# Performance work log

Measured on AMD Instinct MI355X. Metric: run time of the kernel, lower is better.

Reference implementation:

```python
import jax, jax.numpy as jnp
import numpy as np

N = 200_000   # num_nodes
E = 100_000   # events per direction
D = 128       # memory_dim
F = 128       # event feature dim
T = 128       # time encoding dim


def setup_inputs() -> dict:
    key = jax.random.key(0)
    ks = jax.random.split(key, 12)
    src = jax.random.randint(ks[0], (E,), 0, N)
    dst = jax.random.randint(ks[1], (E,), 0, N)
    t = jax.random.uniform(ks[2], (E,)) * 1000.0
    feat = jax.random.normal(ks[3], (E, F))
    memory = jax.random.normal(ks[4], (N, D)) * 0.1
    last_update = jnp.zeros((N,), dtype=jnp.float32)
    time_w = jax.random.normal(ks[5], (T,)) * 0.1
    time_b = jax.random.normal(ks[6], (T,)) * 0.1
    M = 2 * D + T + F  # message dim = 512
    w_ih = jax.random.normal(ks[7], (3 * D, M)) * 0.02
    w_hh = jax.random.normal(ks[8], (3 * D, D)) * 0.02
    b_ih = jnp.zeros((3 * D,), dtype=jnp.float32)
    b_hh = jnp.zeros((3 * D,), dtype=jnp.float32)
    return {
        "memory": memory, "last_update": last_update, "t": t, "feat": feat,
        "time_w": time_w, "time_b": time_b,
        "w_ih": w_ih, "w_hh": w_hh, "b_ih": b_ih, "b_hh": b_hh,
        "src": src, "dst": dst,
    }


def time_encode(dt, w, b):
    # TGN/TGAT-style cosine time encoding: [E] -> [E, T]
    return jnp.cos(dt[:, None] * w[None, :] + b[None, :])


def gru_cell(x, h, w_ih, w_hh, b_ih, b_hh):
    # Standard torch.nn.GRUCell math (gates ordered r, z, n).
    gi = x @ w_ih.T + b_ih  # [N, 3D]
    gh = h @ w_hh.T + b_hh  # [N, 3D]
    i_r, i_z, i_n = jnp.split(gi, 3, axis=-1)
    h_r, h_z, h_n = jnp.split(gh, 3, axis=-1)
    r = jax.nn.sigmoid(i_r + h_r)
    z = jax.nn.sigmoid(i_z + h_z)
    n = jnp.tanh(i_n + r * h_n)
    return (1.0 - z) * n + z * h


def reference(memory, last_update, t, feat, time_w, time_b,
              w_ih, w_hh, b_ih, b_hh, src, dst):
    # --- message functions (identity = concat), both directions ---
    s_msg = jnp.concatenate(
        [memory[src], memory[dst], time_encode(t - last_update[src], time_w, time_b), feat], axis=-1)
    d_msg = jnp.concatenate(
        [memory[dst], memory[src], time_encode(t - last_update[dst], time_w, time_b), feat], axis=-1)

    nodes = jnp.concatenate([src, dst], axis=0)        # [2E]
    te = jnp.concatenate([t, t], axis=0)               # [2E]
    msg = jnp.concatenate([s_msg, d_msg], axis=0)      # [2E, M]

    # --- 'last' aggregator: per-node argmax over event time (scatter_max) ---
    # Stable sort by time; segment_max over sorted positions yields, per node,
    # the latest event (ties broken toward the later original index).
    perm = jnp.argsort(te, stable=True)                # [2E]
    pos = jnp.arange(2 * E)
    best_pos = jax.ops.segment_max(pos, nodes[perm], num_segments=N)  # [N], intmin if empty
    has_msg = best_pos >= 0
    best = perm[jnp.clip(best_pos, 0)]                 # [N] event index of latest msg

    agg_msg = msg[best]                                # [N, M] gather
    max_t = te[best]                                   # [N]

    # --- GRU memory update + masked scatter back into memory ---
    new_mem = gru_cell(agg_msg, memory, w_ih, w_hh, b_ih, b_hh)
    new_memory = jnp.where(has_msg[:, None], new_mem, memory)
    new_last_update = jnp.where(has_msg, max_t, last_update)
    return new_memory, new_last_update
```

## Files before the change

kernel.cpp:

```cpp
#include <hip/hip_runtime.h>
#include <hip/hip_bf16.h>
#include <stdint.h>

typedef __hip_bfloat16 bf16;
typedef unsigned long long u64;
typedef unsigned int u32;
typedef short short8 __attribute__((ext_vector_type(8)));
typedef float f32x4 __attribute__((ext_vector_type(4)));

#define D_ 128
#define K_ 640
#define BM 64
#define BN 128
#define BK 64
#define BM2 32

__device__ __forceinline__ float bf2f(bf16 v) { return __bfloat162float(v); }
__device__ __forceinline__ u32 fbits(float f) { union { float f; u32 u; } c; c.f = f; return c.u; }
__device__ __forceinline__ u32 pk2(float a, float b) {
  union { bf16 h; unsigned short s; } x, y;
  x.h = __float2bfloat16(a); y.h = __float2bfloat16(b);
  return (u32)x.s | ((u32)y.s << 16);
}
template<bool F32>
__device__ __forceinline__ float ldE(const void* p, size_t i) {
  return F32 ? ((const float*)p)[i] : bf2f(((const bf16*)p)[i]);
}
template<bool F32>
__device__ __forceinline__ void stE(void* p, size_t i, float v) {
  if (F32) ((float*)p)[i] = v; else ((bf16*)p)[i] = __float2bfloat16(v);
}
template<bool F32>
__device__ __forceinline__ uint4 ld8(const void* base, size_t elemOff) {
  if (!F32) {
    return *(const uint4*)((const bf16*)base + elemOff);
  } else {
    const float4* p = (const float4*)((const float*)base + elemOff);
    float4 v0 = p[0], v1 = p[1];
    uint4 o; o.x = pk2(v0.x, v0.y); o.y = pk2(v0.z, v0.w);
    o.z = pk2(v1.x, v1.y); o.w = pk2(v1.z, v1.w);
    return o;
  }
}
template<bool F32>
__device__ __forceinline__ void stage8(const void* base, size_t elemOff, bf16* dst) {
  *(uint4*)dst = ld8<F32>(base, elemOff);
}
__device__ __forceinline__ void gl_lds16(const void* g, void* l) {
  __builtin_amdgcn_global_load_lds(
      (const __attribute__((address_space(1))) unsigned int*)g,
      (__attribute__((address_space(3))) unsigned int*)l, 16, 0, 0);
}

__global__ void k_prep(u64* __restrict__ key, u32* __restrict__ cnt, int N,
                       const u32* __restrict__ mem_w, const u32* __restrict__ t_w,
                       u32* __restrict__ flag) {
  int i = blockIdx.x * blockDim.x + threadIdx.x;
  if (i < N) key[i] = 0ull;
  if (i == 0) {
    *cnt = 0u;
    int ok = 1;
    for (int k = 0; k < 64; ++k) {
      u32 w = mem_w[k];
      if ((w & 0x7fffu) > 0x4300u) ok = 0;
      if (((w >> 16) & 0x7fffu) > 0x4300u) ok = 0;
    }
    for (int k = 0; k < 16; ++k) {
      u32 w = t_w[k];
      if ((w & 0xffffu) > 0x4480u) ok = 0;
      if ((w >> 16) > 0x4480u) ok = 0;
    }
    *flag = ok ? 0u : 1u;
  }
}

__global__ void k_scat(const int* __restrict__ src, const int* __restrict__ dst,
                       const void* __restrict__ t, const u32* __restrict__ flag,
                       u64* __restrict__ key, int E) {
  int i = blockIdx.x * blockDim.x + threadIdx.x;
  if (i >= 2 * E) return;
  int e = (i < E) ? i : i - E;
  int node = (i < E) ? src[e] : dst[e];
  float tv = (*flag) ? ((const float*)t)[e] : bf2f(((const bf16*)t)[e]);
  u64 k = ((u64)fbits(tv) << 32) | (u64)(u32)(i + 1);
  atomicMax(&key[node], k);
}

__global__ void k_pack(const void* __restrict__ wih, const void* __restrict__ whh,
                       const u32* __restrict__ flag, bf16* __restrict__ wpk) {
  int gid = blockIdx.x * 256 + threadIdx.x;
  if (gid >= 40960) return;
  int tile = gid >> 10, r = gid & 1023;
  int j = r >> 3, s = r & 7;
  int kc = tile >> 2, by = tile & 3;
  int kglob = kc * 64 + s * 8;
  int grp = j >> 5, gi = j & 31, gidx = 32 * by + gi;
  int srow = (grp == 0) ? gidx : (grp == 1) ? 128 + gidx : 256 + gidx;
  bool zero = (kglob < 512) ? (grp == 3) : (grp == 2);
  uint4 v;
  if (zero) v = (uint4){0u, 0u, 0u, 0u};
  else if (*flag) v = (kglob < 512) ? ld8<true>(wih, (size_t)srow * 512 + kglob)
                                    : ld8<true>(whh, (size_t)srow * 128 + (kglob - 512));
  else            v = (kglob < 512) ? ld8<false>(wih, (size_t)srow * 512 + kglob)
                                    : ld8<false>(whh, (size_t)srow * 128 + (kglob - 512));
  ((uint4*)wpk)[(size_t)tile * 1024 + ((j * 8 + s) ^ (j & 7))] = v;
}

template<bool F32>
__device__ __forceinline__ void compact_body(int n, const void* mem, const void* lastup,
                                             const void* t, const u64* key,
                                             int* list, u32* cnt, int use_list,
                                             void* out, int N, int E) {
  u32 b = (u32)key[n];
  if (b) {
    int pos = (int)(b - 1u);
    int e = (pos < E) ? pos : pos - E;
    stE<F32>(out, (size_t)N * D_ + n, ldE<F32>(t, e));
    if (use_list) { u32 idx = atomicAdd(cnt, 1u); list[idx] = n; }
  } else {
    if (F32) {
      const float4* s = (const float4*)((const float*)mem + (size_t)n * D_);
      float4* d = (float4*)((float*)out + (size_t)n * D_);
#pragma unroll
      for (int i = 0; i < 32; ++i) d[i] = s[i];
    } else {
      const uint4* s = (const uint4*)((const bf16*)mem + (size_t)n * D_);
      uint4* d = (uint4*)((bf16*)out + (size_t)n * D_);
#pragma unroll
      for (int i = 0; i < 16; ++i) d[i] = s[i];
    }
    stE<F32>(out, (size_t)N * D_ + n, ldE<F32>(lastup, n));
  }
}
__global__ void k_compact(const void* mem, const void* lastup, const void* t,
                          const u32* __restrict__ flag, const u64* __restrict__ key,
                          int* list, u32* cnt, int use_list,
                          void* out, int N, int E) {
  int n = blockIdx.x * blockDim.x + threadIdx.x;
  if (n >= N) return;
  if (*flag) compact_body<true>(n, mem, lastup, t, key, list, cnt, use_list, out, N, E);
  else       compact_body<false>(n, mem, lastup, t, key, list, cnt, use_list, out, N, E);
}

template<bool F32>
__device__ __forceinline__ uint4 a_fetch(int kc, int tid,
    const void* mem, const void* feat,
    const int* s_node, const int* s_e, const int* s_oth,
    const float* s_dt, const float* s_tw, const float* s_tb) {
  int r = tid >> 3, s = tid & 7;
  int k0 = kc * 64 + s * 8;
  if (k0 < 128) return ld8<F32>(mem, (size_t)s_node[r] * D_ + k0);
  if (k0 < 256) return ld8<F32>(mem, (size_t)s_oth[r] * D_ + (k0 - 128));
  if (k0 < 384) {
    float dtv = s_dt[r];
    float f[8];
#pragma unroll
    for (int q = 0; q < 8; ++q) {
      int j = k0 - 256 + q;
      f[q] = cosf(fmaf(dtv, s_tw[j], s_tb[j]));
    }
    uint4 o; o.x = pk2(f[0], f[1]); o.y = pk2(f[2], f[3]);
    o.z = pk2(f[4], f[5]); o.w = pk2(f[6], f[7]);
    return o;
  }
  if (k0 < 512) return ld8<F32>(feat, (size_t)s_e[r] * D_ + (k0 - 384));
  return ld8<F32>(mem, (size_t)s_node[r] * D_ + (k0 - 512));
}

__device__ __forceinline__ void b_issue(const bf16* __restrict__ wpk, int tile,
                                        bf16* BsBuf, int tid) {
  int w = tid >> 6;
  const bf16* g = wpk + (size_t)tile * 8192 + w * 2048 + (tid & 63) * 8;
  bf16* l = BsBuf + w * 2048;
#pragma unroll
  for (int i = 0; i < 4; ++i)
    gl_lds16(g + i * 512, l + i * 512);
}

template<bool F32>
__device__ __forceinline__ void gemm2_body(
    const void* mem, const void* lastup, const void* t, const void* feat,
    const int* __restrict__ src, const int* __restrict__ dst,
    const bf16* __restrict__ wpk,
    const void* bih, const void* bhh, const void* tw, const void* tb,
    const u64* __restrict__ key, const int* __restrict__ list,
    const u32* __restrict__ cnt, int use_list,
    void* out, int N, int E,
    char* smem, int* s_node, int* s_e, int* s_oth, int* s_act,
    float* s_dt, float* s_tw, float* s_tb) {
  const int tid = threadIdx.x;
  const int bx = blockIdx.x;
  bf16 (*As)[BM2][72] = (bf16 (*)[BM2][72])smem;
  bf16* BsBase = (bf16*)(smem + 9216);
  float (*Gs)[133] = (float (*)[133])smem;

  b_issue(wpk, 0, BsBase, tid);

  if (tid < BM2) {
    int r = tid, row = BM2 * bx + r, node = -1;
    if (use_list) { int c = (int)*cnt; if (row < c) node = list[row]; }
    else if (row < N) node = row;
    int act = 0, e = 0, oth = 0; float dtv = 0.f;
    if (node >= 0) {
      u32 b = (u32)key[node];
      if (b) {
        act = 1;
        int pos = (int)(b - 1u);
        if (pos < E) { e = pos; oth = dst[e]; } else { e = pos - E; oth = src[e]; }
        dtv = ldE<F32>(t, e) - ldE<F32>(lastup, node);
      }
    }
    if (node < 0) node = 0;
    s_node[r] = node; s_e[r] = e; s_oth[r] = oth; s_act[r] = act; s_dt[r] = dtv;
  }
  if (tid < 128) s_tw[tid] = ldE<F32>(tw, tid);
  else           s_tb[tid - 128] = ldE<F32>(tb, tid - 128);
  __syncthreads();

  {
    uint4 a0 = a_fetch<F32>(0, tid, mem, feat, s_node, s_e, s_oth, s_dt, s_tw, s_tb);
    *(uint4*)&As[0][tid >> 3][(tid & 7) * 8] = a0;
  }
  __syncthreads();

  const int w = tid >> 6, l = tid & 63;
  const int mrow = l & 15, quad = l >> 4;
  f32x4 acc[4][2][2];
#pragma unroll
  for (int by = 0; by < 4; ++by)
#pragma unroll
    for (int mi = 0; mi < 2; ++mi)
#pragma unroll
      for (int ni = 0; ni < 2; ++ni) acc[by][mi][ni] = (f32x4){0.f, 0.f, 0.f, 0.f};

  uint4 apre = (uint4){0u, 0u, 0u, 0u};
#pragma unroll 1
  for (int kc = 0; kc < K_ / 64; ++kc) {
    const int ka = kc & 1;
    short8 a[2][2];
#pragma unroll
    for (int by = 0; by < 4; ++by) {
      const int tile = kc * 4 + by;
      if (by == 0) {
        if (kc + 1 < 10)
          apre = a_fetch<F32>(kc + 1, tid, mem, feat, s_node, s_e, s_oth, s_dt, s_tw, s_tb);
      }
      if (tile + 1 < 40)
        b_issue(wpk, tile + 1, BsBase + (((by & 1) ^ 1) << 13), tid);
      if (by == 0) {
#pragma unroll
        for (int ks2 = 0; ks2 < 2; ++ks2)
#pragma unroll
          for (int mi = 0; mi < 2; ++mi)
            a[ks2][mi] = *(const short8*)((const char*)&As[ka][0][0] +
                             (16 * mi + mrow) * 144 + ks2 * 64 + quad * 16);
      }
      const char* Bsb = (const char*)(BsBase + ((by & 1) << 13));
      short8 b[2][2];
#pragma unroll
      for (int ks2 = 0; ks2 < 2; ++ks2)
#pragma unroll
        for (int ni = 0; ni < 2; ++ni) {
          int j = 32 * w + 16 * ni + mrow;
          int off = (j * 128 + ks2 * 64 + quad * 16) ^ ((j & 7) << 4);
          b[ks2][ni] = *(const short8*)(Bsb + off);
        }
#pragma unroll
      for (int ks2 = 0; ks2 < 2; ++ks2)
#pragma unroll
        for (int mi = 0; mi < 2; ++mi)
#pragma unroll
          for (int ni = 0; ni < 2; ++ni)
            acc[by][mi][ni] = __builtin_amdgcn_mfma_f32_16x16x32_bf16(
                a[ks2][mi], b[ks2][ni], acc[by][mi][ni], 0, 0, 0);
      if (by == 3 && kc + 1 < 10)
        *(uint4*)&As[ka ^ 1][tid >> 3][(tid & 7) * 8] = apre;
      __syncthreads();
    }
  }

#pragma unroll
  for (int by = 0; by < 4; ++by) {
#pragma unroll
    for (int mi = 0; mi < 2; ++mi)
#pragma unroll
      for (int ni = 0; ni < 2; ++ni)
#pragma unroll
        for (int reg = 0; reg < 4; ++reg)
          Gs[16 * mi + quad * 4 + reg][32 * w + 16 * ni + mrow] = acc[by][mi][ni][reg];
    __syncthreads();
    {
      int r = tid >> 3, giB = (tid & 7) * 4;
      if (s_act[r]) {
        int node = s_node[r];
#pragma unroll
        for (int q = 0; q < 4; ++q) {
          int gi = giB + q, gidx = 32 * by + gi;
          float rp  = Gs[r][gi]      + ldE<F32>(bih, gidx)       + ldE<F32>(bhh, gidx);
          float zp  = Gs[r][32 + gi] + ldE<F32>(bih, 128 + gidx) + ldE<F32>(bhh, 128 + gidx);
          float inp = Gs[r][64 + gi] + ldE<F32>(bih, 256 + gidx);
          float hnp = Gs[r][96 + gi] + ldE<F32>(bhh, 256 + gidx);
          float rg = 1.f / (1.f + expf(-rp));
          float zg = 1.f / (1.f + expf(-zp));
          float ng = tanhf(inp + rg * hnp);
          float h = ldE<F32>(mem, (size_t)node * D_ + gidx);
          stE<F32>(out, (size_t)node * D_ + gidx, (1.f - zg) * ng + zg * h);
        }
      }
    }
    __syncthreads();
  }
}

__global__ __launch_bounds__(256, 3)
void k_gemm2(const void* mem, const void* lastup, const void* t, const void* feat,
             const int* src, const int* dst, const bf16* wpk,
             const void* bih, const void* bhh, const void* tw, const void* tb,
             const u32* __restrict__ flag, const u64* __restrict__ key,
             const int* __restrict__ list, const u32* __restrict__ cnt, int use_list,
             void* out, int N, int E) {
  if (use_list && (int)*cnt <= BM2 * (int)blockIdx.x) return;
  __shared__ __align__(16) char smem[41984];
  __shared__ int s_node[BM2], s_e[BM2], s_oth[BM2], s_act[BM2];
  __shared__ float s_dt[BM2], s_tw[128], s_tb[128];
  if (*flag)
    gemm2_body<true>(mem, lastup, t, feat, src, dst, wpk, bih, bhh, tw, tb,
                     key, list, cnt, use_list, out, N, E,
                     smem, s_node, s_e, s_oth, s_act, s_dt, s_tw, s_tb);
  else
    gemm2_body<false>(mem, lastup, t, feat, src, dst, wpk, bih, bhh, tw, tb,
                      key, list, cnt, use_list, out, N, E,
                      smem, s_node, s_e, s_oth, s_act, s_dt, s_tw, s_tb);
}

template<bool F32>
__device__ __forceinline__ void gemm_body(
    const void* mem, const void* lastup, const void* t, const void* feat,
    const int* __restrict__ src, const int* __restrict__ dst,
    const void* wih, const void* whh, const void* bih, const void* bhh,
    const void* tw, const void* tb,
    const u64* __restrict__ key, const int* __restrict__ list,
    const u32* __restrict__ cnt, int use_list,
    void* out, int N, int E,
    bf16 (*As)[72], bf16 (*Bs)[72], float (*Gs)[132],
    int* s_node, int* s_e, int* s_oth, int* s_act, float* s_dt) {
  const int tid = threadIdx.x;
  const int bx = blockIdx.x, by = blockIdx.y;

  if (tid < BM) {
    int r = tid;
    int row = BM * bx + r;
    int node = -1;
    if (use_list) { int c = (int)*cnt; if (row < c) node = list[row]; }
    else if (row < N) node = row;
    int act = 0, e = 0, oth = 0; float dtv = 0.f;
    if (node >= 0) {
      u32 b = (u32)key[node];
      if (b) {
        act = 1;
        int pos = (int)(b - 1u);
        if (pos < E) { e = pos; oth = dst[e]; } else { e = pos - E; oth = src[e]; }
        dtv = ldE<F32>(t, e) - ldE<F32>(lastup, node);
      }
    }
    if (node < 0) node = 0;
    s_node[r] = node; s_e[r] = e; s_oth[r] = oth; s_act[r] = act; s_dt[r] = dtv;
  }

  const int w = tid >> 6, l = tid & 63;
  const int mrow = l & 15, quad = l >> 4;
  f32x4 acc[4][2];
#pragma unroll
  for (int mi = 0; mi < 4; ++mi)
#pragma unroll
    for (int ni = 0; ni < 2; ++ni) acc[mi][ni] = (f32x4){0.f, 0.f, 0.f, 0.f};

#pragma unroll 1
  for (int kc = 0; kc < K_ / BK; ++kc) {
    __syncthreads();
#pragma unroll
    for (int it = 0; it < 2; ++it) {
      int task = tid + 256 * it;
      int r = task >> 3, s = task & 7;
      int k0 = kc * BK + s * 8;
      bf16* dstp = &As[r][s * 8];
      if (k0 < 128)       stage8<F32>(mem,  (size_t)s_node[r] * D_ + k0, dstp);
      else if (k0 < 256)  stage8<F32>(mem,  (size_t)s_oth[r] * D_ + (k0 - 128), dstp);
      else if (k0 < 384) {
        float dtv = s_dt[r];
        float f[8];
#pragma unroll
        for (int q = 0; q < 8; ++q) {
          int j = k0 - 256 + q;
          f[q] = cosf(fmaf(dtv, ldE<F32>(tw, j), ldE<F32>(tb, j)));
        }
        uint4 o; o.x = pk2(f[0], f[1]); o.y = pk2(f[2], f[3]);
        o.z = pk2(f[4], f[5]); o.w = pk2(f[6], f[7]);
        *(uint4*)dstp = o;
      }
      else if (k0 < 512)  stage8<F32>(feat, (size_t)s_e[r] * D_ + (k0 - 384), dstp);
      else                stage8<F32>(mem,  (size_t)s_node[r] * D_ + (k0 - 512), dstp);
    }
#pragma unroll
    for (int it = 0; it < 4; ++it) {
      int task = tid + 256 * it;
      int j = task >> 3, s = task & 7;
      int k0 = kc * BK + s * 8;
      int grp = j >> 5, gi = j & 31;
      int gidx = 32 * by + gi;
      bf16* dstp = &Bs[j][s * 8];
      if (k0 < 512) {
        if (grp == 3) { *(uint4*)dstp = (uint4){0, 0, 0, 0}; }
        else {
          int srow = (grp == 0) ? gidx : (grp == 1) ? 128 + gidx : 256 + gidx;
          stage8<F32>(wih, (size_t)srow * 512 + k0, dstp);
        }
      } else {
        if (grp == 2) { *(uint4*)dstp = (uint4){0, 0, 0, 0}; }
        else {
          int srow = (grp == 0) ? gidx : (grp == 1) ? 128 + gidx : 256 + gidx;
          stage8<F32>(whh, (size_t)srow * D_ + (k0 - 512), dstp);
        }
      }
    }
    __syncthreads();
#pragma unroll
    for (int ks = 0; ks < BK; ks += 32) {
      short8 a[4], b[2];
#pragma unroll
      for (int mi = 0; mi < 4; ++mi)
        a[mi] = *(const short8*)&As[16 * mi + mrow][ks + quad * 8];
#pragma unroll
      for (int ni = 0; ni < 2; ++ni)
        b[ni] = *(const short8*)&Bs[32 * w + 16 * ni + mrow][ks + quad * 8];
#pragma unroll
      for (int mi = 0; mi < 4; ++mi)
#pragma unroll
        for (int ni = 0; ni < 2; ++ni)
          acc[mi][ni] = __builtin_amdgcn_mfma_f32_16x16x32_bf16(a[mi], b[ni], acc[mi][ni], 0, 0, 0);
    }
  }

#pragma unroll
  for (int mi = 0; mi < 4; ++mi)
#pragma unroll
    for (int ni = 0; ni < 2; ++ni)
#pragma unroll
      for (int reg = 0; reg < 4; ++reg)
        Gs[16 * mi + quad * 4 + reg][32 * w + 16 * ni + mrow] = acc[mi][ni][reg];
  __syncthreads();

  {
    int r = tid >> 2;
    int giB = (tid & 3) * 8;
    if (s_act[r]) {
      int node = s_node[r];
#pragma unroll
      for (int q = 0; q < 8; ++q) {
        int gi = giB + q;
        int gidx = 32 * by + gi;
        float rp  = Gs[r][gi]       + ldE<F32>(bih, gidx)       + ldE<F32>(bhh, gidx);
        float zp  = Gs[r][32 + gi]  + ldE<F32>(bih, 128 + gidx) + ldE<F32>(bhh, 128 + gidx);
        float inp = Gs[r][64 + gi]  + ldE<F32>(bih, 256 + gidx);
        float hnp = Gs[r][96 + gi]  + ldE<F32>(bhh, 256 + gidx);
        float rg = 1.f / (1.f + expf(-rp));
        float zg = 1.f / (1.f + expf(-zp));
        float ng = tanhf(inp + rg * hnp);
        float h = ldE<F32>(mem, (size_t)node * D_ + gidx);
        stE<F32>(out, (size_t)node * D_ + gidx, (1.f - zg) * ng + zg * h);
      }
    }
  }
}

__global__ __launch_bounds__(256)
void k_gemm_fb(const void* mem, const void* lastup, const void* t, const void* feat,
               const int* src, const int* dst,
               const void* wih, const void* whh, const void* bih, const void* bhh,
               const void* tw, const void* tb,
               const u32* __restrict__ flag, const u64* __restrict__ key,
               const int* __restrict__ list, const u32* __restrict__ cnt, int use_list,
               void* out, int N, int E) {
  if (use_list && (int)*cnt <= BM * (int)blockIdx.x) return;

  __shared__ __align__(16) bf16 As[BM][72];
  __shared__ __align__(16) bf16 Bs[BN][72];
  __shared__ __align__(16) float Gs[BM][132];
  __shared__ int s_node[BM], s_e[BM], s_oth[BM], s_act[BM];
  __shared__ float s_dt[BM];

  if (*flag)
    gemm_body<true>(mem, lastup, t, feat, src, dst, wih, whh, bih, bhh, tw, tb,
                    key, list, cnt, use_list, out, N, E,
                    As, Bs, Gs, s_node, s_e, s_oth, s_act, s_dt);
  else
    gemm_body<false>(mem, lastup, t, feat, src, dst, wih, whh, bih, bhh, tw, tb,
                     key, list, cnt, use_list, out, N, E,
                     As, Bs, Gs, s_node, s_e, s_oth, s_act, s_dt);
}

extern "C" void kernel_launch(void* const* d_in, const int* in_sizes, int n_in,
                              void* d_out, int out_size, void* d_ws, size_t ws_size,
                              hipStream_t stream) {
  const void* mem    = d_in[0];
  const void* lastup = d_in[1];
  const void* t      = d_in[2];
  const void* feat   = d_in[3];
  const void* tw     = d_in[4];
  const void* tb     = d_in[5];
  const void* wih    = d_in[6];
  const void* whh    = d_in[7];
  const void* bih    = d_in[8];
  const void* bhh    = d_in[9];
  const int*  src    = (const int*)d_in[10];
  const int*  dst    = (const int*)d_in[11];

  int N = in_sizes[0] / D_;
  int E = in_sizes[2];

  char* ws = (char*)d_ws;
  size_t off = 0;
  u32* flag = (u32*)(ws + off); off += 16;
  u32* cnt  = (u32*)(ws + off); off += 16;
  u64* key  = (u64*)(ws + off); off += (size_t)N * 8;
  int* list = (int*)(ws + off); off += (size_t)N * 4;
  int use_list = (ws_size >= off) ? 1 : 0;
  bf16* wpk = (bf16*)(ws + off); off += (size_t)512 * 640 * 2;
  int use_wpk = (ws_size >= off) ? 1 : 0;

  const int thr = 256;
  int nb  = (N + thr - 1) / thr;
  int eb  = (2 * E + thr - 1) / thr;

  k_prep<<<dim3(nb), dim3(thr), 0, stream>>>(key, cnt, N, (const u32*)mem, (const u32*)t, flag);
  k_scat<<<dim3(eb), dim3(thr), 0, stream>>>(src, dst, t, flag, key, E);
  if (use_wpk)
    k_pack<<<dim3(160), dim3(thr), 0, stream>>>(wih, whh, flag, wpk);
  k_compact<<<dim3(nb), dim3(thr), 0, stream>>>(mem, lastup, t, flag, key,
                                                list, cnt, use_list, d_out, N, E);
  if (use_wpk) {
    int mt = (N + BM2 - 1) / BM2;
    k_gemm2<<<dim3(mt), dim3(thr), 0, stream>>>(
        mem, lastup, t, feat, src, dst, wpk, bih, bhh, tw, tb,
        flag, key, list, cnt, use_list, d_out, N, E);
  } else {
    int mt = (N + BM - 1) / BM;
    k_gemm_fb<<<dim3(mt, 4), dim3(thr), 0, stream>>>(
        mem, lastup, t, feat, src, dst, wih, whh, bih, bhh, tw, tb,
        flag, key, list, cnt, use_list, d_out, N, E);
  }
}
```

Baseline: 516.8 us.

## Triple-buffer weight tiles with vmcnt waits and warp-aggregated compaction atomics

Moves the GEMM B-tile prefetch from double to triple buffering, issuing two tiles ahead and replacing most per-tile __syncthreads with explicit vmcnt waits plus one barrier per K chunk. The A-operand fetch is split into raw load and later pack so that fp32 conversion happens after the loads land. It also raises MFMA priority with setprio. The compaction kernel now uses one ballot-based atomic per block instead of one atomic per active node. The cost is more LDS and occupancy lowered from 3 to 2 blocks, and the hand-tuned vmcnt counts are fragile.

After: 550.9 us. 1.07x slower.

```diff
diff --git a/kernel.cpp b/kernel.cpp
--- a/kernel.cpp
+++ b/kernel.cpp
@@ -14,6 +14,8 @@
 #define BN 128
 #define BK 64
 #define BM2 32
+
+#define VMWAIT(n) asm volatile("s_waitcnt vmcnt(" #n ")" ::: "memory")
 
 __device__ __forceinline__ float bf2f(bf16 v) { return __bfloat162float(v); }
 __device__ __forceinline__ u32 fbits(float f) { union { float f; u32 u; } c; c.f = f; return c.u; }
@@ -107,16 +109,36 @@
 }
 
 template<bool F32>
-__device__ __forceinline__ void compact_body(int n, const void* mem, const void* lastup,
+__device__ __forceinline__ void compact_body(int n, bool nvalid,
+                                             const void* mem, const void* lastup,
                                              const void* t, const u64* key,
                                              int* list, u32* cnt, int use_list,
-                                             void* out, int N, int E) {
-  u32 b = (u32)key[n];
-  if (b) {
+                                             void* out, int N, int E, u32* s_wb) {
+  u32 b = 0;
+  if (nvalid) b = (u32)key[n];
+  bool active = nvalid && (b != 0u);
+  if (use_list) {
+    u64 mask = __ballot(active);
+    int lane = threadIdx.x & 63, w = threadIdx.x >> 6;
+    if (lane == 0) s_wb[w] = (u32)__popcll(mask);
+    __syncthreads();
+    if (threadIdx.x == 0) {
+      u32 tot = s_wb[0] + s_wb[1] + s_wb[2] + s_wb[3];
+      u32 base = tot ? atomicAdd(cnt, tot) : 0u;
+      u32 acc0 = base;
+      for (int i = 0; i < 4; ++i) { u32 c = s_wb[i]; s_wb[i] = acc0; acc0 += c; }
+    }
+    __syncthreads();
+    if (active) {
+      u32 idx = s_wb[w] + (u32)__popcll(mask & ((1ull << lane) - 1ull));
+      list[idx] = n;
+    }
+  }
+  if (!nvalid) return;
+  if (active) {
     int pos = (int)(b - 1u);
     int e = (pos < E) ? pos : pos - E;
     stE<F32>(out, (size_t)N * D_ + n, ldE<F32>(t, e));
-    if (use_list) { u32 idx = atomicAdd(cnt, 1u); list[idx] = n; }
   } else {
     if (F32) {
       const float4* s = (const float4*)((const float*)mem + (size_t)n * D_);
@@ -136,22 +158,24 @@
                           const u32* __restrict__ flag, const u64* __restrict__ key,
                           int* list, u32* cnt, int use_list,
                           void* out, int N, int E) {
+  __shared__ u32 s_wb[4];
   int n = blockIdx.x * blockDim.x + threadIdx.x;
-  if (n >= N) return;
-  if (*flag) compact_body<true>(n, mem, lastup, t, key, list, cnt, use_list, out, N, E);
-  else       compact_body<false>(n, mem, lastup, t, key, list, cnt, use_list, out, N, E);
-}
-
-template<bool F32>
-__device__ __forceinline__ uint4 a_fetch(int kc, int tid,
+  bool nvalid = (n < N);
+  if (*flag) compact_body<true>(n, nvalid, mem, lastup, t, key, list, cnt, use_list, out, N, E, s_wb);
+  else       compact_body<false>(n, nvalid, mem, lastup, t, key, list, cnt, use_list, out, N, E, s_wb);
+}
+
+struct AR { uint4 lo, hi; };
+
+template<bool F32>
+__device__ __forceinline__ AR a_fetch_raw(int kcn, int tid,
     const void* mem, const void* feat,
     const int* s_node, const int* s_e, const int* s_oth,
     const float* s_dt, const float* s_tw, const float* s_tb) {
   int r = tid >> 3, s = tid & 7;
-  int k0 = kc * 64 + s * 8;
-  if (k0 < 128) return ld8<F32>(mem, (size_t)s_node[r] * D_ + k0);
-  if (k0 < 256) return ld8<F32>(mem, (size_t)s_oth[r] * D_ + (k0 - 128));
-  if (k0 < 384) {
+  int k0 = kcn * 64 + s * 8;
+  AR a;
+  if (k0 >= 256 && k0 < 384) {
     float dtv = s_dt[r];
     float f[8];
 #pragma unroll
@@ -159,12 +183,34 @@
       int j = k0 - 256 + q;
       f[q] = cosf(fmaf(dtv, s_tw[j], s_tb[j]));
     }
-    uint4 o; o.x = pk2(f[0], f[1]); o.y = pk2(f[2], f[3]);
-    o.z = pk2(f[4], f[5]); o.w = pk2(f[6], f[7]);
-    return o;
-  }
-  if (k0 < 512) return ld8<F32>(feat, (size_t)s_e[r] * D_ + (k0 - 384));
-  return ld8<F32>(mem, (size_t)s_node[r] * D_ + (k0 - 512));
+    a.lo.x = pk2(f[0], f[1]); a.lo.y = pk2(f[2], f[3]);
+    a.lo.z = pk2(f[4], f[5]); a.lo.w = pk2(f[6], f[7]);
+    a.hi = a.lo;
+    return a;
+  }
+  const void* base = mem;
+  size_t eo;
+  if (k0 < 128)       eo = (size_t)s_node[r] * D_ + k0;
+  else if (k0 < 256)  eo = (size_t)s_oth[r] * D_ + (k0 - 128);
+  else if (k0 < 512) { base = feat; eo = (size_t)s_e[r] * D_ + (k0 - 384); }
+  else                eo = (size_t)s_node[r] * D_ + (k0 - 512);
+  if (F32) {
+    const uint4* p = (const uint4*)((const float*)base + eo);
+    a.lo = p[0]; a.hi = p[1];
+  } else {
+    a.lo = *(const uint4*)((const bf16*)base + eo);
+    a.hi = a.lo;
+  }
+  return a;
+}
+template<bool F32>
+__device__ __forceinline__ uint4 a_pack(AR a, int kcn) {
+  if (!F32) return a.lo;
+  if (kcn == 4 || kcn == 5) return a.lo;
+  union { uint4 u; float4 f; } l, h; l.u = a.lo; h.u = a.hi;
+  uint4 o; o.x = pk2(l.f.x, l.f.y); o.y = pk2(l.f.z, l.f.w);
+  o.z = pk2(h.f.x, h.f.y); o.w = pk2(h.f.z, h.f.w);
+  return o;
 }
 
 __device__ __forceinline__ void b_issue(const bf16* __restrict__ wpk, int tile,
@@ -195,6 +241,7 @@
   float (*Gs)[133] = (float (*)[133])smem;
 
   b_issue(wpk, 0, BsBase, tid);
+  b_issue(wpk, 1, BsBase + 8192, tid);
 
   if (tid < BM2) {
     int r = tid, row = BM2 * bx + r, node = -1;
@@ -218,10 +265,11 @@
   __syncthreads();
 
   {
-    uint4 a0 = a_fetch<F32>(0, tid, mem, feat, s_node, s_e, s_oth, s_dt, s_tw, s_tb);
-    *(uint4*)&As[0][tid >> 3][(tid & 7) * 8] = a0;
-  }
-  __syncthreads();
+    AR a0 = a_fetch_raw<F32>(0, tid, mem, feat, s_node, s_e, s_oth, s_dt, s_tw, s_tb);
+    *(uint4*)&As[0][tid >> 3][(tid & 7) * 8] = a_pack<F32>(a0, 0);
+  }
+  asm volatile("s_waitcnt lgkmcnt(0)" ::: "memory");
+  __builtin_amdgcn_s_barrier();
 
   const int w = tid >> 6, l = tid & 63;
   const int mrow = l & 15, quad = l >> 4;
@@ -233,20 +281,27 @@
 #pragma unroll
       for (int ni = 0; ni < 2; ++ni) acc[by][mi][ni] = (f32x4){0.f, 0.f, 0.f, 0.f};
 
-  uint4 apre = (uint4){0u, 0u, 0u, 0u};
+  int bc = 0;
 #pragma unroll 1
-  for (int kc = 0; kc < K_ / 64; ++kc) {
+  for (int kc = 0; kc < 10; ++kc) {
     const int ka = kc & 1;
+    const bool hasA = (kc + 1 < 10) & (kc + 1 != 4) & (kc + 1 != 5);
     short8 a[2][2];
+    AR apre;
 #pragma unroll
     for (int by = 0; by < 4; ++by) {
       const int tile = kc * 4 + by;
-      if (by == 0) {
-        if (kc + 1 < 10)
-          apre = a_fetch<F32>(kc + 1, tid, mem, feat, s_node, s_e, s_oth, s_dt, s_tw, s_tb);
-      }
-      if (tile + 1 < 40)
-        b_issue(wpk, tile + 1, BsBase + (((by & 1) ^ 1) << 13), tid);
+      int bi = bc + 2; if (bi >= 3) bi -= 3;
+      if (tile + 2 < 40) b_issue(wpk, tile + 2, BsBase + bi * 8192, tid);
+      if (by == 0 && kc + 1 < 10)
+        apre = a_fetch_raw<F32>(kc + 1, tid, mem, feat, s_node, s_e, s_oth, s_dt, s_tw, s_tb);
+      if (by < 3) {
+        if (kc == 9)      { if (by < 2) VMWAIT(8); else VMWAIT(4); }
+        else if (hasA)    { if (F32) VMWAIT(10); else VMWAIT(9); }
+        else              VMWAIT(8);
+      } else {
+        if (kc == 9) VMWAIT(0); else VMWAIT(8);
+      }
       if (by == 0) {
 #pragma unroll
         for (int ks2 = 0; ks2 < 2; ++ks2)
@@ -255,7 +310,7 @@
             a[ks2][mi] = *(const short8*)((const char*)&As[ka][0][0] +
                              (16 * mi + mrow) * 144 + ks2 * 64 + quad * 16);
       }
-      const char* Bsb = (const char*)(BsBase + ((by & 1) << 13));
+      const char* Bsb = (const char*)(BsBase + bc * 8192);
       short8 b[2][2];
 #pragma unroll
       for (int ks2 = 0; ks2 < 2; ++ks2)
@@ -265,6 +320,7 @@
           int off = (j * 128 + ks2 * 64 + quad * 16) ^ ((j & 7) << 4);
           b[ks2][ni] = *(const short8*)(Bsb + off);
         }
+      __builtin_amdgcn_s_setprio(1);
 #pragma unroll
       for (int ks2 = 0; ks2 < 2; ++ks2)
 #pragma unroll
@@ -273,9 +329,14 @@
           for (int ni = 0; ni < 2; ++ni)
             acc[by][mi][ni] = __builtin_amdgcn_mfma_f32_16x16x32_bf16(
                 a[ks2][mi], b[ks2][ni], acc[by][mi][ni], 0, 0, 0);
-      if (by == 3 && kc + 1 < 10)
-        *(uint4*)&As[ka ^ 1][tid >> 3][(tid & 7) * 8] = apre;
-      __syncthreads();
+      __builtin_amdgcn_s_setprio(0);
+      if (by == 3) {
+        if (kc + 1 < 10)
+          *(uint4*)&As[ka ^ 1][tid >> 3][(tid & 7) * 8] = a_pack<F32>(apre, kc + 1);
+        asm volatile("s_waitcnt lgkmcnt(0)" ::: "memory");
+        __builtin_amdgcn_s_barrier();
+      }
+      bc = (bc + 1 == 3) ? 0 : bc + 1;
     }
   }
 
@@ -312,7 +373,7 @@
   }
 }
 
-__global__ __launch_bounds__(256, 3)
+__global__ __launch_bounds__(256, 2)
 void k_gemm2(const void* mem, const void* lastup, const void* t, const void* feat,
              const int* src, const int* dst, const bf16* wpk,
              const void* bih, const void* bhh, const void* tw, const void* tb,
@@ -320,7 +381,7 @@
              const int* __restrict__ list, const u32* __restrict__ cnt, int use_list,
              void* out, int N, int E) {
   if (use_list && (int)*cnt <= BM2 * (int)blockIdx.x) return;
-  __shared__ __align__(16) char smem[41984];
+  __shared__ __align__(16) char smem[58368];
   __shared__ int s_node[BM2], s_e[BM2], s_oth[BM2], s_act[BM2];
   __shared__ float s_dt[BM2], s_tw[128], s_tb[128];
   if (*flag)
```

## Fold hidden-state weights into input GEMM and stream operands directly to registers

Applied to the files above, without the earlier changes.

The weight packing now pre-adds w_hh into the w_ih columns for the r and z gates, since the aggregated message already contains the node's own memory. That shrinks the reduction from 640 to 512, and the n-gate hidden term gets its own reduced slice. The GEMM drops its LDS staging and barriers: B tiles are loaded in MFMA fragment layout straight into registers with a triple buffer, and A fragments are gathered per lane, with the cosine time encoding computed in registers. Compaction uses wave-ballot prefix sums so each block does one atomic instead of one per active node. The risks are higher register pressure, uncoalesced per-lane gathers, and bf16 rounding of the summed weights.

New measurement: 1.819 ms. 3.52x slower.

```diff
diff --git a/kernel.cpp b/kernel.cpp
--- a/kernel.cpp
+++ b/kernel.cpp
@@ -9,11 +9,10 @@
 typedef float f32x4 __attribute__((ext_vector_type(4)));
 
 #define D_ 128
-#define K_ 640
 #define BM 64
 #define BN 128
 #define BK 64
-#define BM2 32
+#define KFB 640
 
 __device__ __forceinline__ float bf2f(bf16 v) { return __bfloat162float(v); }
 __device__ __forceinline__ u32 fbits(float f) { union { float f; u32 u; } c; c.f = f; return c.u; }
@@ -22,6 +21,8 @@
   x.h = __float2bfloat16(a); y.h = __float2bfloat16(b);
   return (u32)x.s | ((u32)y.s << 16);
 }
+union U4S8 { uint4 u; short8 s; };
+__device__ __forceinline__ short8 u2s(uint4 v) { U4S8 c; c.u = v; return c.s; }
 template<bool F32>
 __device__ __forceinline__ float ldE(const void* p, size_t i) {
   return F32 ? ((const float*)p)[i] : bf2f(((const bf16*)p)[i]);
@@ -45,11 +46,6 @@
 template<bool F32>
 __device__ __forceinline__ void stage8(const void* base, size_t elemOff, bf16* dst) {
   *(uint4*)dst = ld8<F32>(base, elemOff);
-}
-__device__ __forceinline__ void gl_lds16(const void* g, void* l) {
-  __builtin_amdgcn_global_load_lds(
-      (const __attribute__((address_space(1))) unsigned int*)g,
-      (__attribute__((address_space(3))) unsigned int*)l, 16, 0, 0);
 }
 
 __global__ void k_prep(u64* __restrict__ key, u32* __restrict__ cnt, int N,
@@ -86,37 +82,71 @@
   atomicMax(&key[node], k);
 }
 
-__global__ void k_pack(const void* __restrict__ wih, const void* __restrict__ whh,
-                       const u32* __restrict__ flag, bf16* __restrict__ wpk) {
-  int gid = blockIdx.x * 256 + threadIdx.x;
-  if (gid >= 40960) return;
-  int tile = gid >> 10, r = gid & 1023;
-  int j = r >> 3, s = r & 7;
+__global__ void k_pack3(const void* __restrict__ wih, const void* __restrict__ whh,
+                        const u32* __restrict__ flag, bf16* __restrict__ wpk) {
+  int g = blockIdx.x * 256 + threadIdx.x;
+  if (g >= 32768) return;
+  int tile = g >> 10, sub = (g >> 6) & 15, lane = g & 63;
+  int w = sub >> 2, ks2 = (sub >> 1) & 1, ni = sub & 1;
+  int mrow = lane & 15, quad = lane >> 4;
+  int j = 32 * w + 16 * ni + mrow;
+  int kk = ks2 * 32 + quad * 8;
   int kc = tile >> 2, by = tile & 3;
-  int kglob = kc * 64 + s * 8;
+  int kglob = kc * 64 + kk;
   int grp = j >> 5, gi = j & 31, gidx = 32 * by + gi;
-  int srow = (grp == 0) ? gidx : (grp == 1) ? 128 + gidx : 256 + gidx;
-  bool zero = (kglob < 512) ? (grp == 3) : (grp == 2);
-  uint4 v;
-  if (zero) v = (uint4){0u, 0u, 0u, 0u};
-  else if (*flag) v = (kglob < 512) ? ld8<true>(wih, (size_t)srow * 512 + kglob)
-                                    : ld8<true>(whh, (size_t)srow * 128 + (kglob - 512));
-  else            v = (kglob < 512) ? ld8<false>(wih, (size_t)srow * 512 + kglob)
-                                    : ld8<false>(whh, (size_t)srow * 128 + (kglob - 512));
-  ((uint4*)wpk)[(size_t)tile * 1024 + ((j * 8 + s) ^ (j & 7))] = v;
-}
-
-template<bool F32>
-__device__ __forceinline__ void compact_body(int n, const void* mem, const void* lastup,
+  bool F = (*flag != 0);
+  float f[8];
+#pragma unroll
+  for (int q = 0; q < 8; ++q) {
+    int k = kglob + q;
+    float v = 0.f;
+    if (grp < 3) {
+      int srow = grp * 128 + gidx;
+      v = F ? ldE<true>(wih, (size_t)srow * 512 + k) : ldE<false>(wih, (size_t)srow * 512 + k);
+      if (k < 128 && grp < 2)
+        v += F ? ldE<true>(whh, (size_t)srow * 128 + k) : ldE<false>(whh, (size_t)srow * 128 + k);
+    } else if (k < 128) {
+      v = F ? ldE<true>(whh, (size_t)(256 + gidx) * 128 + k)
+            : ldE<false>(whh, (size_t)(256 + gidx) * 128 + k);
+    }
+    f[q] = v;
+  }
+  uint4 o; o.x = pk2(f[0], f[1]); o.y = pk2(f[2], f[3]);
+  o.z = pk2(f[4], f[5]); o.w = pk2(f[6], f[7]);
+  ((uint4*)wpk)[g] = o;
+}
+
+template<bool F32>
+__device__ __forceinline__ void compact_body(int n, bool nvalid,
+                                             const void* mem, const void* lastup,
                                              const void* t, const u64* key,
                                              int* list, u32* cnt, int use_list,
-                                             void* out, int N, int E) {
-  u32 b = (u32)key[n];
-  if (b) {
+                                             void* out, int N, int E, u32* s_wb) {
+  u32 b = 0;
+  if (nvalid) b = (u32)key[n];
+  bool active = nvalid && (b != 0u);
+  if (use_list) {
+    u64 mask = __ballot(active);
+    int lane = threadIdx.x & 63, w = threadIdx.x >> 6;
+    if (lane == 0) s_wb[w] = (u32)__popcll(mask);
+    __syncthreads();
+    if (threadIdx.x == 0) {
+      u32 tot = s_wb[0] + s_wb[1] + s_wb[2] + s_wb[3];
+      u32 base = tot ? atomicAdd(cnt, tot) : 0u;
+      u32 acc0 = base;
+      for (int i = 0; i < 4; ++i) { u32 c = s_wb[i]; s_wb[i] = acc0; acc0 += c; }
+    }
+    __syncthreads();
+    if (active) {
+      u32 idx = s_wb[w] + (u32)__popcll(mask & ((1ull << lane) - 1ull));
+      list[idx] = n;
+    }
+  }
+  if (!nvalid) return;
+  if (active) {
     int pos = (int)(b - 1u);
     int e = (pos < E) ? pos : pos - E;
     stE<F32>(out, (size_t)N * D_ + n, ldE<F32>(t, e));
-    if (use_list) { u32 idx = atomicAdd(cnt, 1u); list[idx] = n; }
   } else {
     if (F32) {
       const float4* s = (const float4*)((const float*)mem + (size_t)n * D_);
@@ -136,49 +166,15 @@
                           const u32* __restrict__ flag, const u64* __restrict__ key,
                           int* list, u32* cnt, int use_list,
                           void* out, int N, int E) {
+  __shared__ u32 s_wb[4];
   int n = blockIdx.x * blockDim.x + threadIdx.x;
-  if (n >= N) return;
-  if (*flag) compact_body<true>(n, mem, lastup, t, key, list, cnt, use_list, out, N, E);
-  else       compact_body<false>(n, mem, lastup, t, key, list, cnt, use_list, out, N, E);
-}
-
-template<bool F32>
-__device__ __forceinline__ uint4 a_fetch(int kc, int tid,
-    const void* mem, const void* feat,
-    const int* s_node, const int* s_e, const int* s_oth,
-    const float* s_dt, const float* s_tw, const float* s_tb) {
-  int r = tid >> 3, s = tid & 7;
-  int k0 = kc * 64 + s * 8;
-  if (k0 < 128) return ld8<F32>(mem, (size_t)s_node[r] * D_ + k0);
-  if (k0 < 256) return ld8<F32>(mem, (size_t)s_oth[r] * D_ + (k0 - 128));
-  if (k0 < 384) {
-    float dtv = s_dt[r];
-    float f[8];
-#pragma unroll
-    for (int q = 0; q < 8; ++q) {
-      int j = k0 - 256 + q;
-      f[q] = cosf(fmaf(dtv, s_tw[j], s_tb[j]));
-    }
-    uint4 o; o.x = pk2(f[0], f[1]); o.y = pk2(f[2], f[3]);
-    o.z = pk2(f[4], f[5]); o.w = pk2(f[6], f[7]);
-    return o;
-  }
-  if (k0 < 512) return ld8<F32>(feat, (size_t)s_e[r] * D_ + (k0 - 384));
-  return ld8<F32>(mem, (size_t)s_node[r] * D_ + (k0 - 512));
-}
-
-__device__ __forceinline__ void b_issue(const bf16* __restrict__ wpk, int tile,
-                                        bf16* BsBuf, int tid) {
-  int w = tid >> 6;
-  const bf16* g = wpk + (size_t)tile * 8192 + w * 2048 + (tid & 63) * 8;
-  bf16* l = BsBuf + w * 2048;
-#pragma unroll
-  for (int i = 0; i < 4; ++i)
-    gl_lds16(g + i * 512, l + i * 512);
-}
-
-template<bool F32>
-__device__ __forceinline__ void gemm2_body(
+  bool nvalid = (n < N);
+  if (*flag) compact_body<true>(n, nvalid, mem, lastup, t, key, list, cnt, use_list, out, N, E, s_wb);
+  else       compact_body<false>(n, nvalid, mem, lastup, t, key, list, cnt, use_list, out, N, E, s_wb);
+}
+
+template<bool F32>
+__device__ __forceinline__ void gemm3_body(
     const void* mem, const void* lastup, const void* t, const void* feat,
     const int* __restrict__ src, const int* __restrict__ dst,
     const bf16* __restrict__ wpk,
@@ -186,18 +182,13 @@
     const u64* __restrict__ key, const int* __restrict__ list,
     const u32* __restrict__ cnt, int use_list,
     void* out, int N, int E,
-    char* smem, int* s_node, int* s_e, int* s_oth, int* s_act,
-    float* s_dt, float* s_tw, float* s_tb) {
+    float (*Gs)[132], int* s_node, int* s_e, int* s_oth, int* s_act,
+    float* s_dt, float* s_twb) {
   const int tid = threadIdx.x;
   const int bx = blockIdx.x;
-  bf16 (*As)[BM2][72] = (bf16 (*)[BM2][72])smem;
-  bf16* BsBase = (bf16*)(smem + 9216);
-  float (*Gs)[133] = (float (*)[133])smem;
-
-  b_issue(wpk, 0, BsBase, tid);
-
-  if (tid < BM2) {
-    int r = tid, row = BM2 * bx + r, node = -1;
+
+  if (tid < 32) {
+    int r = tid, row = 32 * bx + r, node = -1;
     if (use_list) { int c = (int)*cnt; if (row < c) node = list[row]; }
     else if (row < N) node = row;
     int act = 0, e = 0, oth = 0; float dtv = 0.f;
@@ -213,18 +204,25 @@
     if (node < 0) node = 0;
     s_node[r] = node; s_e[r] = e; s_oth[r] = oth; s_act[r] = act; s_dt[r] = dtv;
   }
-  if (tid < 128) s_tw[tid] = ldE<F32>(tw, tid);
-  else           s_tb[tid - 128] = ldE<F32>(tb, tid - 128);
-  __syncthreads();
-
-  {
-    uint4 a0 = a_fetch<F32>(0, tid, mem, feat, s_node, s_e, s_oth, s_dt, s_tw, s_tb);
-    *(uint4*)&As[0][tid >> 3][(tid & 7) * 8] = a0;
+  if (tid >= 128) {
+    int i = tid - 128;
+    s_twb[i] = ldE<F32>(tw, i);
+    s_twb[128 + i] = ldE<F32>(tb, i);
   }
   __syncthreads();
 
   const int w = tid >> 6, l = tid & 63;
   const int mrow = l & 15, quad = l >> 4;
+  const bool w3 = (w == 3);
+  const int koq = quad * 8;
+
+  const int nd0 = s_node[mrow],    nd1 = s_node[16 + mrow];
+  const int ot0 = s_oth[mrow],     ot1 = s_oth[16 + mrow];
+  const int ev0 = s_e[mrow],       ev1 = s_e[16 + mrow];
+  const float dt0 = s_dt[mrow],    dt1 = s_dt[16 + mrow];
+
+  uint4 braw[3][4];
+  uint4 alo[2][4];
   f32x4 acc[4][2][2];
 #pragma unroll
   for (int by = 0; by < 4; ++by)
@@ -233,49 +231,92 @@
 #pragma unroll
       for (int ni = 0; ni < 2; ++ni) acc[by][mi][ni] = (f32x4){0.f, 0.f, 0.f, 0.f};
 
-  uint4 apre = (uint4){0u, 0u, 0u, 0u};
-#pragma unroll 1
-  for (int kc = 0; kc < K_ / 64; ++kc) {
-    const int ka = kc & 1;
-    short8 a[2][2];
+  auto BISSUE = [&](int tile_) {
+    const uint4* bp = (const uint4*)wpk + ((size_t)(tile_ * 16 + w * 4)) * 64 + l;
+#pragma unroll
+    for (int f = 0; f < 4; ++f) braw[tile_ % 3][f] = bp[(size_t)f * 64];
+  };
+  auto AROW = [&](int kn, int mi) -> int {
+    return (kn < 2) ? (mi ? nd1 : nd0) : (kn < 4) ? (mi ? ot1 : ot0) : (mi ? ev1 : ev0);
+  };
+  auto ALOADB = [&](int kn) {
+#pragma unroll
+    for (int ks2 = 0; ks2 < 2; ++ks2)
+#pragma unroll
+      for (int mi = 0; mi < 2; ++mi) {
+        const void* base = (kn < 4) ? mem : feat;
+        size_t eo = (size_t)AROW(kn, mi) * D_ + (kn & 1) * 64 + ks2 * 32 + koq;
+        alo[kn & 1][ks2 * 2 + mi] = *(const uint4*)((const bf16*)base + eo);
+      }
+  };
+  auto ALOADF = [&](int kn) {
+#pragma unroll
+    for (int ks2 = 0; ks2 < 2; ++ks2)
+#pragma unroll
+      for (int mi = 0; mi < 2; ++mi) {
+        const void* base = (kn < 4) ? mem : feat;
+        size_t eo = (size_t)AROW(kn, mi) * D_ + (kn & 1) * 64 + ks2 * 32 + koq;
+        const float4* p = (const float4*)((const float*)base + eo);
+        float4 v0 = p[0], v1 = p[1];
+        uint4 o; o.x = pk2(v0.x, v0.y); o.y = pk2(v0.z, v0.w);
+        o.z = pk2(v1.x, v1.y); o.w = pk2(v1.z, v1.w);
+        alo[kn & 1][ks2 * 2 + mi] = o;
+      }
+  };
+  auto ACOS = [&](int kc_) {
+#pragma unroll
+    for (int ks2 = 0; ks2 < 2; ++ks2) {
+      int kbase = (kc_ - 4) * 64 + ks2 * 32 + koq;
+      float tv[8], bv[8];
+#pragma unroll
+      for (int e2 = 0; e2 < 8; ++e2) { tv[e2] = s_twb[kbase + e2]; bv[e2] = s_twb[128 + kbase + e2]; }
+#pragma unroll
+      for (int mi = 0; mi < 2; ++mi) {
+        float dtv = mi ? dt1 : dt0;
+        u32 p[4];
+#pragma unroll
+        for (int e2 = 0; e2 < 4; ++e2)
+          p[e2] = pk2(cosf(fmaf(dtv, tv[2 * e2], bv[2 * e2])),
+                      cosf(fmaf(dtv, tv[2 * e2 + 1], bv[2 * e2 + 1])));
+        alo[kc_ & 1][ks2 * 2 + mi] = (uint4){p[0], p[1], p[2], p[3]};
+      }
+    }
+  };
+
+  BISSUE(0);
+  if (F32) ; else ALOADB(0);
+  BISSUE(1);
+
+#pragma unroll
+  for (int kc = 0; kc < 8; ++kc) {
 #pragma unroll
     for (int by = 0; by < 4; ++by) {
-      const int tile = kc * 4 + by;
+      const int tt = kc * 4 + by;
+      if (tt + 2 < 32 && !(w3 && (tt + 2) >= 8)) BISSUE(tt + 2);
       if (by == 0) {
-        if (kc + 1 < 10)
-          apre = a_fetch<F32>(kc + 1, tid, mem, feat, s_node, s_e, s_oth, s_dt, s_tw, s_tb);
-      }
-      if (tile + 1 < 40)
-        b_issue(wpk, tile + 1, BsBase + (((by & 1) ^ 1) << 13), tid);
-      if (by == 0) {
+        if (!(w3 && kc >= 2)) {
+          if (kc == 4 || kc == 5) ACOS(kc);
+          else if (F32) ALOADF(kc);
+        }
+        if (!F32) {
+          const int kn = kc + 1;
+          if ((kn == 1 || kn == 2 || kn == 3 || kn == 6 || kn == 7) && !(w3 && kn >= 2))
+            ALOADB(kn);
+        }
+      }
+      if (!(w3 && kc >= 2)) {
+        __builtin_amdgcn_s_setprio(1);
 #pragma unroll
         for (int ks2 = 0; ks2 < 2; ++ks2)
 #pragma unroll
           for (int mi = 0; mi < 2; ++mi)
-            a[ks2][mi] = *(const short8*)((const char*)&As[ka][0][0] +
-                             (16 * mi + mrow) * 144 + ks2 * 64 + quad * 16);
-      }
-      const char* Bsb = (const char*)(BsBase + ((by & 1) << 13));
-      short8 b[2][2];
-#pragma unroll
-      for (int ks2 = 0; ks2 < 2; ++ks2)
-#pragma unroll
-        for (int ni = 0; ni < 2; ++ni) {
-          int j = 32 * w + 16 * ni + mrow;
-          int off = (j * 128 + ks2 * 64 + quad * 16) ^ ((j & 7) << 4);
-          b[ks2][ni] = *(const short8*)(Bsb + off);
-        }
-#pragma unroll
-      for (int ks2 = 0; ks2 < 2; ++ks2)
-#pragma unroll
-        for (int mi = 0; mi < 2; ++mi)
-#pragma unroll
-          for (int ni = 0; ni < 2; ++ni)
-            acc[by][mi][ni] = __builtin_amdgcn_mfma_f32_16x16x32_bf16(
-                a[ks2][mi], b[ks2][ni], acc[by][mi][ni], 0, 0, 0);
-      if (by == 3 && kc + 1 < 10)
-        *(uint4*)&As[ka ^ 1][tid >> 3][(tid & 7) * 8] = apre;
-      __syncthreads();
+#pragma unroll
+            for (int ni = 0; ni < 2; ++ni)
+              acc[by][mi][ni] = __builtin_amdgcn_mfma_f32_16x16x32_bf16(
+                  u2s(alo[kc & 1][ks2 * 2 + mi]), u2s(braw[tt % 3][ks2 * 2 + ni]),
+                  acc[by][mi][ni], 0, 0, 0);
+        __builtin_amdgcn_s_setprio(0);
+      }
     }
   }
 
@@ -313,24 +354,24 @@
 }
 
 __global__ __launch_bounds__(256, 3)
-void k_gemm2(const void* mem, const void* lastup, const void* t, const void* feat,
+void k_gemm3(const void* mem, const void* lastup, const void* t, const void* feat,
              const int* src, const int* dst, const bf16* wpk,
              const void* bih, const void* bhh, const void* tw, const void* tb,
              const u32* __restrict__ flag, const u64* __restrict__ key,
              const int* __restrict__ list, const u32* __restrict__ cnt, int use_list,
              void* out, int N, int E) {
-  if (use_list && (int)*cnt <= BM2 * (int)blockIdx.x) return;
-  __shared__ __align__(16) char smem[41984];
-  __shared__ int s_node[BM2], s_e[BM2], s_oth[BM2], s_act[BM2];
-  __shared__ float s_dt[BM2], s_tw[128], s_tb[128];
+  if (use_list && (int)*cnt <= 32 * (int)blockIdx.x) return;
+  __shared__ float Gs[32][132];
+  __shared__ int s_node[32], s_e[32], s_oth[32], s_act[32];
+  __shared__ float s_dt[32], s_twb[256];
   if (*flag)
-    gemm2_body<true>(mem, lastup, t, feat, src, dst, wpk, bih, bhh, tw, tb,
+    gemm3_body<true>(mem, lastup, t, feat, src, dst, wpk, bih, bhh, tw, tb,
                      key, list, cnt, use_list, out, N, E,
-                     smem, s_node, s_e, s_oth, s_act, s_dt, s_tw, s_tb);
+                     Gs, s_node, s_e, s_oth, s_act, s_dt, s_twb);
   else
-    gemm2_body<false>(mem, lastup, t, feat, src, dst, wpk, bih, bhh, tw, tb,
+    gemm3_body<false>(mem, lastup, t, feat, src, dst, wpk, bih, bhh, tw, tb,
                       key, list, cnt, use_list, out, N, E,
-                      smem, s_node, s_e, s_oth, s_act, s_dt, s_tw, s_tb);
+                      Gs, s_node, s_e, s_oth, s_act, s_dt, s_twb);
 }
 
 template<bool F32>
@@ -376,7 +417,7 @@
     for (int ni = 0; ni < 2; ++ni) acc[mi][ni] = (f32x4){0.f, 0.f, 0.f, 0.f};
 
 #pragma unroll 1
-  for (int kc = 0; kc < K_ / BK; ++kc) {
+  for (int kc = 0; kc < KFB / BK; ++kc) {
     __syncthreads();
 #pragma unroll
     for (int it = 0; it < 2; ++it) {
@@ -525,23 +566,23 @@
   u64* key  = (u64*)(ws + off); off += (size_t)N * 8;
   int* list = (int*)(ws + off); off += (size_t)N * 4;
   int use_list = (ws_size >= off) ? 1 : 0;
-  bf16* wpk = (bf16*)(ws + off); off += (size_t)512 * 640 * 2;
-  int use_wpk = (ws_size >= off) ? 1 : 0;
+  bf16* wpk3 = (bf16*)(ws + off); off += (size_t)512 * 512 * 2;
+  int use3 = (ws_size >= off) ? 1 : 0;
 
   const int thr = 256;
-  int nb  = (N + thr - 1) / thr;
-  int eb  = (2 * E + thr - 1) / thr;
+  int nb = (N + thr - 1) / thr;
+  int eb = (2 * E + thr - 1) / thr;
 
   k_prep<<<dim3(nb), dim3(thr), 0, stream>>>(key, cnt, N, (const u32*)mem, (const u32*)t, flag);
   k_scat<<<dim3(eb), dim3(thr), 0, stream>>>(src, dst, t, flag, key, E);
-  if (use_wpk)
-    k_pack<<<dim3(160), dim3(thr), 0, stream>>>(wih, whh, flag, wpk);
+  if (use3)
+    k_pack3<<<dim3(128), dim3(thr), 0, stream>>>(wih, whh, flag, wpk3);
   k_compact<<<dim3(nb), dim3(thr), 0, stream>>>(mem, lastup, t, flag, key,
                                                 list, cnt, use_list, d_out, N, E);
-  if (use_wpk) {
-    int mt = (N + BM2 - 1) / BM2;
-    k_gemm2<<<dim3(mt), dim3(thr), 0, stream>>>(
-        mem, lastup, t, feat, src, dst, wpk, bih, bhh, tw, tb,
+  if (use3) {
+    int mt = (N + 31) / 32;
+    k_gemm3<<<dim3(mt), dim3(thr), 0, stream>>>(
+        mem, lastup, t, feat, src, dst, wpk3, bih, bhh, tw, tb,
         flag, key, list, cnt, use_list, d_out, N, E);
   } else {
     int mt = (N + BM - 1) / BM;
```
